# Performance work log

Hardware: AMD Instinct MI355X
Metric: run time of the kernel (lower is better)

Reference implementation:

```python
import math
import jax, jax.numpy as jnp
import numpy as np

B, H, W, C = 4, 64, 64, 96
SSM_RATIO = 2.0
D_INNER = int(SSM_RATIO * C)   # 192
D_STATE = 4
DT_RANK = math.ceil(C / 16)    # 6
K = 4                          # 4 scan directions
D_CONV = 3


def layer_norm(x, g, b, eps=1e-5):
    mu = jnp.mean(x, axis=-1, keepdims=True)
    var = jnp.var(x, axis=-1, keepdims=True)
    return (x - mu) / jnp.sqrt(var + eps) * g + b


def cross_scan(x):
    # x: (B, D, H, W) -> (B, K=4, D, L); dirs: row-major, col-major, and their reverses
    b, d, h, w = x.shape
    s0 = x.reshape(b, d, h * w)
    s1 = jnp.transpose(x, (0, 1, 3, 2)).reshape(b, d, h * w)
    return jnp.stack([s0, s1, s0[..., ::-1], s1[..., ::-1]], axis=1)


def cross_merge(ys, h, w):
    # ys: (B, K=4, D, L) -> (B, D, L); inverse of cross_scan, summed over directions
    b, k, d, L = ys.shape
    ys = ys[:, 0:2] + ys[:, 2:4][..., ::-1]
    y0 = ys[:, 0]
    y1 = jnp.transpose(ys[:, 1].reshape(b, d, w, h), (0, 1, 3, 2)).reshape(b, d, L)
    return y0 + y1


def selective_scan(u, dt, A, Bm, Cm, D4):
    # u, dt: (B,K,D,L); A: (K,D,N); Bm, Cm: (B,K,N,L); D4: (K,D)
    u_l = jnp.moveaxis(u, -1, 0)    # (L,B,K,D)
    dt_l = jnp.moveaxis(dt, -1, 0)
    B_l = jnp.moveaxis(Bm, -1, 0)   # (L,B,K,N)
    C_l = jnp.moveaxis(Cm, -1, 0)

    def step(h, inp):
        u_t, dt_t, B_t, C_t = inp
        dA = jnp.exp(dt_t[..., None] * A)                              # (B,K,D,N)
        h = h * dA + dt_t[..., None] * B_t[:, :, None, :] * u_t[..., None]
        y = jnp.sum(h * C_t[:, :, None, :], axis=-1)                   # (B,K,D)
        return h, y

    h0 = jnp.zeros(u.shape[:3] + (A.shape[-1],), u.dtype)
    _, ys = jax.lax.scan(step, h0, (u_l, dt_l, B_l, C_l))
    return jnp.moveaxis(ys, 0, -1) + D4[None, :, :, None] * u


def _block(x_rgb, x_e, in_proj_x_w, in_proj_e_w, conv_x_w, conv_x_b, conv_e_w, conv_e_b,
           x_proj_weight, dt_projs_weight, dt_projs_bias, A_logs, Ds,
           ln_r_g, ln_r_b, ln_e_g, ln_e_b, out_proj_x_w, out_proj_e_w):
    b, h, w, c = x_rgb.shape
    Din, N, R = D_INNER, D_STATE, DT_RANK

    xr = jnp.einsum('bhwc,dc->bhwd', x_rgb, in_proj_x_w)
    xe = jnp.einsum('bhwc,dc->bhwd', x_e, in_proj_e_w)
    xr = jnp.transpose(xr, (0, 3, 1, 2))  # (B,Din,H,W)
    xe = jnp.transpose(xe, (0, 3, 1, 2))

    def dwconv(x, wt, bias):
        y = jax.lax.conv_general_dilated(x, wt, (1, 1), 'SAME', feature_group_count=Din)
        return jax.nn.silu(y + bias[None, :, None, None])

    xr = dwconv(xr, conv_x_w, conv_x_b)
    xe = dwconv(xe, conv_e_w, conv_e_b)

    xs_r = cross_scan(xr)  # (B,K,Din,L)
    xs_e = cross_scan(xe)

    def proj(xs):
        dbl = jnp.einsum('bkdl,kcd->bkcl', xs, x_proj_weight)
        dtl, Bm, Cm = dbl[:, :, :R], dbl[:, :, R:R + N], dbl[:, :, R + N:]
        dtl = jnp.einsum('bkrl,kdr->bkdl', dtl, dt_projs_weight)
        dtl = jax.nn.softplus(dtl + dt_projs_bias[None, :, :, None])
        return dtl, Bm, Cm

    dt_r, B_r, C_r = proj(xs_r)
    dt_e, B_e, C_e = proj(xs_e)

    A = -jnp.exp(A_logs).reshape(K, Din, N)
    D4 = Ds.reshape(K, Din)

    # cross fusion: each modality's scan reads out through the OTHER modality's C
    y_r = selective_scan(xs_r, dt_r, A, B_r, C_e, D4)
    y_e = selective_scan(xs_e, dt_e, A, B_e, C_r, D4)

    y_r = cross_merge(y_r, h, w)  # (B,Din,L)
    y_e = cross_merge(y_e, h, w)

    y_r = layer_norm(jnp.transpose(y_r, (0, 2, 1)), ln_r_g, ln_r_b).reshape(b, h, w, Din)
    y_e = layer_norm(jnp.transpose(y_e, (0, 2, 1)), ln_e_g, ln_e_b).reshape(b, h, w, Din)

    out_r = jnp.einsum('bhwd,cd->bhwc', y_r, out_proj_x_w)
    out_e = jnp.einsum('bhwd,cd->bhwc', y_e, out_proj_e_w)

    # residual add of the wrapping block (drop_path=0, mlp_ratio=0)
    return x_rgb + out_r, x_e + out_e


def setup_inputs():
    key = jax.random.key(0)
    ks = jax.random.split(key, 16)
    N, R, Din = D_STATE, DT_RANK, D_INNER

    def rn(k, shape, s=0.02):
        return (jax.random.normal(k, shape) * s).astype(jnp.float32)

    # dt bias: inverse-softplus of dt ~ U[1e-3, 0.1]  (mamba-style init)
    dt = jnp.exp(jax.random.uniform(ks[10], (K, Din)) * (np.log(0.1) - np.log(1e-3)) + np.log(1e-3))
    dt_bias = dt + jnp.log(-jnp.expm1(-dt))

    return {
        'x_rgb': jax.random.normal(ks[0], (B, H, W, C), jnp.float32),
        'x_e': jax.random.normal(ks[1], (B, H, W, C), jnp.float32),
        'in_proj_x_w': rn(ks[2], (Din, C)),
        'in_proj_e_w': rn(ks[3], (Din, C)),
        'conv_x_w': rn(ks[4], (Din, 1, D_CONV, D_CONV), 0.1),
        'conv_x_b': jnp.zeros((Din,), jnp.float32),
        'conv_e_w': rn(ks[5], (Din, 1, D_CONV, D_CONV), 0.1),
        'conv_e_b': jnp.zeros((Din,), jnp.float32),
        'x_proj_weight': rn(ks[6], (K, R + 2 * N, Din)),
        'dt_projs_weight': rn(ks[7], (K, Din, R), R ** -0.5),
        'dt_projs_bias': dt_bias.astype(jnp.float32),
        'A_logs': jnp.log(jnp.tile(jnp.arange(1, N + 1, dtype=jnp.float32), (K * Din, 1))),
        'Ds': jnp.ones((K * Din,), jnp.float32),
        'ln_r_g': jnp.ones((Din,), jnp.float32),
        'ln_r_b': jnp.zeros((Din,), jnp.float32),
        'ln_e_g': jnp.ones((Din,), jnp.float32),
        'ln_e_b': jnp.zeros((Din,), jnp.float32),
        'out_proj_x_w': rn(ks[8], (C, Din)),
        'out_proj_e_w': rn(ks[9], (C, Din)),
    }


def reference(x_rgb, x_e, in_proj_x_w, in_proj_e_w, conv_x_w, conv_x_b, conv_e_w, conv_e_b,
              x_proj_weight, dt_projs_weight, dt_projs_bias, A_logs, Ds,
              ln_r_g, ln_r_b, ln_e_g, ln_e_b, out_proj_x_w, out_proj_e_w):
    return _block(x_rgb, x_e, in_proj_x_w, in_proj_e_w, conv_x_w, conv_x_b, conv_e_w, conv_e_b,
                  x_proj_weight, dt_projs_weight, dt_projs_bias, A_logs, Ds,
                  ln_r_g, ln_r_b, ln_e_g, ln_e_b, out_proj_x_w, out_proj_e_w)
```

## Files before the change

### kernel.cpp

```cpp
#include <hip/hip_runtime.h>

#define BB 4
#define HH 64
#define WW 64
#define CC 96
#define DIN 192
#define NS 4
#define RR 6
#define KK 4
#define LL 4096
#define NPOS (BB*LL)
#define NPD ((size_t)NPOS*DIN)
#define NDBC ((size_t)BB*KK*LL*14)
#define NCHUNK 128
#define CLEN 32
#define NCHAIN 32
#define PB 8

__device__ __forceinline__ int map_pos(int k, int l){
  switch(k){
    case 0: return l;
    case 1: { int wi=l>>6, hi=l&63; return hi*WW+wi; }
    case 2: return LL-1-l;
    default:{ int lr=LL-1-l; int wi=lr>>6, hi=lr&63; return hi*WW+wi; }
  }
}
__device__ __forceinline__ int pos_stride(int k){
  return (k==0) ? 1 : (k==1) ? WW : (k==2) ? -1 : -WW;
}

__global__ __launch_bounds__(DIN) void inproj_kernel(
    const float* __restrict__ x_rgb, const float* __restrict__ x_e,
    const float* __restrict__ w_r,   const float* __restrict__ w_e,
    float* __restrict__ xproj_r,    float* __restrict__ xproj_e){
  int blk = blockIdx.x;
  int m = blk / (NPOS/PB); int g = blk % (NPOS/PB);
  size_t rem0 = (size_t)g * PB;
  const float* x = m ? x_e : x_rgb;
  const float* w = m ? w_e : w_r;
  float* o = m ? xproj_e : xproj_r;
  __shared__ float xs[PB][CC];
  __shared__ float wt[DIN][17];
  int t = threadIdx.x;
  for(int idx=t; idx<PB*CC; idx+=DIN) xs[idx/CC][idx%CC] = x[rem0*CC + idx];
  float acc[PB];
  #pragma unroll
  for(int p=0;p<PB;p++) acc[p]=0.f;
  for(int c0=0; c0<CC; c0+=16){
    __syncthreads();
    for(int idx=t; idx<DIN*16; idx+=DIN){
      int dd = idx>>4, cc = idx&15;
      wt[dd][cc] = w[(size_t)dd*CC + c0 + cc];
    }
    __syncthreads();
    #pragma unroll
    for(int cc=0; cc<16; cc++){
      float wv = wt[t][cc];
      #pragma unroll
      for(int p=0;p<PB;p++) acc[p] += xs[p][c0+cc]*wv;
    }
  }
  #pragma unroll
  for(int p=0;p<PB;p++) o[(rem0+p)*DIN + t] = acc[p];
}

__global__ __launch_bounds__(DIN) void conv_kernel(
    const float* __restrict__ xproj_r, const float* __restrict__ xproj_e,
    const float* __restrict__ cw_r, const float* __restrict__ cb_r,
    const float* __restrict__ cw_e, const float* __restrict__ cb_e,
    float* __restrict__ xconv_r, float* __restrict__ xconv_e){
  int blk = blockIdx.x;
  int m = blk / NPOS; int rem = blk % NPOS;
  int b = rem / LL, p = rem % LL;
  int y = p >> 6, x = p & 63;
  const float* in = (m ? xproj_e : xproj_r) + (size_t)b*LL*DIN;
  const float* cw = m ? cw_e : cw_r;
  const float* cb = m ? cb_e : cb_r;
  float* out = m ? xconv_e : xconv_r;
  int d = threadIdx.x;
  float acc = cb[d];
  #pragma unroll
  for(int dy=-1;dy<=1;dy++){
    int yy = y+dy; if(yy<0 || yy>=HH) continue;
    #pragma unroll
    for(int dx=-1;dx<=1;dx++){
      int xx = x+dx; if(xx<0 || xx>=WW) continue;
      acc += in[(size_t)(yy*WW+xx)*DIN + d] * cw[d*9 + (dy+1)*3 + (dx+1)];
    }
  }
  float s = acc / (1.f + __expf(-acc));
  out[(size_t)(b*LL+p)*DIN + d] = s;
}

#define TPOS 32
__global__ __launch_bounds__(256) void projbc_kernel(
    const float* __restrict__ xconv_r, const float* __restrict__ xconv_e,
    const float* __restrict__ xpw,
    float* __restrict__ dtBC_r, float* __restrict__ dtBC_e){
  int blk = blockIdx.x;
  int m = blk / (BB*LL/TPOS); int rem = blk % (BB*LL/TPOS);
  int b = rem / (LL/TPOS); int p0 = (rem % (LL/TPOS)) * TPOS;
  const float* xc = (m ? xconv_e : xconv_r) + ((size_t)b*LL + p0)*DIN;
  float* o = (m ? dtBC_e : dtBC_r) + (size_t)b*KK*LL*14;

  __shared__ float xs[TPOS*97];
  __shared__ float wsd[56*97];

  int t = threadIdx.x;
  int g = t >> 5;
  int pl = t & 31;

  float acc[7];
  #pragma unroll
  for(int j=0;j<7;j++) acc[j]=0.f;

  for(int dt0=0; dt0<DIN; dt0+=96){
    __syncthreads();
    for(int idx=t; idx<TPOS*96; idx+=256){
      int r = idx/96, ccol = idx%96;
      xs[r*97+ccol] = xc[(size_t)r*DIN + dt0 + ccol];
    }
    for(int idx=t; idx<56*96; idx+=256){
      int r = idx/96, ccol = idx%96;
      wsd[r*97+ccol] = xpw[(size_t)r*DIN + dt0 + ccol];
    }
    __syncthreads();
    const float* xrow = &xs[pl*97];
    #pragma unroll 4
    for(int d=0; d<96; d++){
      float xv = xrow[d];
      #pragma unroll
      for(int j=0;j<7;j++) acc[j] += wsd[(g*7+j)*97 + d]*xv;
    }
  }

  int p = p0 + pl;
  int ptr_ = (p&63)*64 + (p>>6);
  #pragma unroll
  for(int j=0;j<7;j++){
    int cbar = g*7+j;
    int k = cbar/14, c = cbar%14;
    int l = (k==0) ? p : (k==1) ? ptr_ : (k==2) ? (LL-1-p) : (LL-1-ptr_);
    o[((size_t)k*LL + l)*14 + c] = acc[j];
  }
}

__global__ __launch_bounds__(DIN) void scan_p1_kernel(
    const float* __restrict__ xconv_r, const float* __restrict__ xconv_e,
    const float* __restrict__ dtBC_r, const float* __restrict__ dtBC_e,
    const float* __restrict__ dtw, const float* __restrict__ dtb,
    const float* __restrict__ A_logs,
    float* __restrict__ trans_S, float* __restrict__ sumdt){
  int ch = blockIdx.x / NCHUNK;
  int cidx = blockIdx.x % NCHUNK;
  int m = ch >> 4, b = (ch>>2)&3, k = ch&3;
  int d = threadIdx.x;
  int l0 = cidx*CLEN;

  float4 al = *(const float4*)&A_logs[(size_t)(k*DIN+d)*NS];
  float A0=-__expf(al.x), A1=-__expf(al.y), A2=-__expf(al.z), A3=-__expf(al.w);
  float Wd[RR];
  #pragma unroll
  for(int r=0;r<RR;r++) Wd[r] = dtw[((size_t)k*DIN + d)*RR + r];
  float bias = dtb[k*DIN+d];

  const float* xc    = (m ? xconv_e : xconv_r) + (size_t)b*LL*DIN;
  const float* dbc_m = (m ? dtBC_e : dtBC_r) + ((size_t)b*KK + k)*LL*14;

  __shared__ float4 db4[CLEN][4];
  __shared__ float u_s[CLEN*DIN];
  float* dbf = (float*)db4;

  for(int idx=d; idx<CLEN*14; idx+=DIN){
    int i = idx/14, j = idx%14;
    int slot = (j<6) ? (8+j) : (j-6);
    dbf[i*16+slot] = dbc_m[(size_t)l0*14 + idx];
  }
  int stride = pos_stride(k);
  int pos0 = map_pos(k, l0);
  #pragma unroll 8
  for(int i=0;i<CLEN;i++)
    u_s[i*DIN+d] = xc[(size_t)(pos0+i*stride)*DIN + d];
  __syncthreads();

  float h0=0.f,h1=0.f,h2=0.f,h3=0.f,sd=0.f;
  #pragma unroll 4
  for(int i=0;i<CLEN;i++){
    float4 Bv  = db4[i][0];
    float4 d03 = db4[i][2];
    float4 d45 = db4[i][3];
    float dtr = fmaf(d03.x,Wd[0], fmaf(d03.y,Wd[1], fmaf(d03.z,Wd[2],
                fmaf(d03.w,Wd[3], fmaf(d45.x,Wd[4], fmaf(d45.y,Wd[5], bias))))));
    float dt = fmaxf(dtr,0.f) + __logf(1.f + __expf(-fabsf(dtr)));
    sd += dt;
    float u = u_s[i*DIN + d];
    float dtu = dt*u;
    h0 = fmaf(h0, __expf(dt*A0), dtu*Bv.x);
    h1 = fmaf(h1, __expf(dt*A1), dtu*Bv.y);
    h2 = fmaf(h2, __expf(dt*A2), dtu*Bv.z);
    h3 = fmaf(h3, __expf(dt*A3), dtu*Bv.w);
  }
  size_t base = ((size_t)(ch*NCHUNK + cidx)*NS)*DIN + d;
  trans_S[base          ] = h0;
  trans_S[base +   DIN  ] = h1;
  trans_S[base + 2*DIN  ] = h2;
  trans_S[base + 3*DIN  ] = h3;
  sumdt[(size_t)(ch*NCHUNK + cidx)*DIN + d] = sd;
}

__global__ __launch_bounds__(DIN) void scan_p2_kernel(
    const float* __restrict__ trans_S, const float* __restrict__ sumdt,
    const float* __restrict__ A_logs, float* __restrict__ hin){
  int ch = blockIdx.x; int k = ch & 3; int d = threadIdx.x;
  float4 al = *(const float4*)&A_logs[(size_t)(k*DIN+d)*NS];
  float A[NS] = {-__expf(al.x), -__expf(al.y), -__expf(al.z), -__expf(al.w)};
  float h[NS] = {0.f,0.f,0.f,0.f};
  for(int c0=0;c0<NCHUNK;c0+=4){
    float S[4][NS], sdv[4];
    #pragma unroll
    for(int cc=0;cc<4;cc++){
      size_t base = ((size_t)(ch*NCHUNK + c0+cc)*NS)*DIN + d;
      #pragma unroll
      for(int n=0;n<NS;n++) S[cc][n] = trans_S[base + (size_t)n*DIN];
      sdv[cc] = sumdt[(size_t)(ch*NCHUNK + c0+cc)*DIN + d];
    }
    #pragma unroll
    for(int cc=0;cc<4;cc++){
      size_t base = ((size_t)(ch*NCHUNK + c0+cc)*NS)*DIN + d;
      #pragma unroll
      for(int n=0;n<NS;n++) hin[base + (size_t)n*DIN] = h[n];
      #pragma unroll
      for(int n=0;n<NS;n++) h[n] = fmaf(h[n], __expf(A[n]*sdv[cc]), S[cc][n]);
    }
  }
}

__global__ __launch_bounds__(DIN) void scan_p3_kernel(
    const float* __restrict__ xconv_r, const float* __restrict__ xconv_e,
    const float* __restrict__ dtBC_r, const float* __restrict__ dtBC_e,
    const float* __restrict__ dtw, const float* __restrict__ dtb,
    const float* __restrict__ A_logs, const float* __restrict__ Ds,
    const float* __restrict__ hin,
    float* __restrict__ ym_a_r, float* __restrict__ ym_a_e,
    float* __restrict__ ym_b_r, float* __restrict__ ym_b_e){
  int blk = blockIdx.x;
  int cidx = blk % NCHUNK;
  int rem  = blk / NCHUNK;
  int pg = rem & 1; rem >>= 1;
  int b  = rem & 3; int m = rem >> 2;
  int kA = pg, kB = pg + 2;
  int cidx2 = NCHUNK-1-cidx;
  int l0A = cidx*CLEN, l0B = cidx2*CLEN;

  int d = threadIdx.x;
  int st = pos_stride(kA);
  int pos0 = map_pos(kA, l0A);

  const float* xc = (m ? xconv_e : xconv_r) + (size_t)b*LL*DIN;
  const float* dbc_own = (m ? dtBC_e : dtBC_r) + (size_t)b*KK*LL*14;
  const float* dbc_oth = (m ? dtBC_r : dtBC_e) + (size_t)b*KK*LL*14;
  float* ym = (pg==0) ? (m ? ym_a_e : ym_a_r) : (m ? ym_b_e : ym_b_r);
  ym += (size_t)b*LL*DIN;

  __shared__ float4 db4A[CLEN][4];
  __shared__ float4 db4B[CLEN][4];
  __shared__ float u_s[CLEN*DIN];
  float* dbfA = (float*)db4A;
  float* dbfB = (float*)db4B;

  for(int idx=d; idx<CLEN*14; idx+=DIN){
    int i = idx/14, j = idx%14;
    int slot = (j<6) ? (8+j) : (j-6);
    dbfA[i*16+slot] = dbc_own[((size_t)kA*LL + l0A)*14 + idx];
    dbfB[i*16+slot] = dbc_own[((size_t)kB*LL + l0B)*14 + idx];
  }
  for(int idx=d; idx<CLEN*NS; idx+=DIN){
    int i = idx>>2, j = idx&3;
    dbfA[i*16 + 4 + j] = dbc_oth[((size_t)kA*LL + l0A + i)*14 + 10 + j];
    dbfB[i*16 + 4 + j] = dbc_oth[((size_t)kB*LL + l0B + i)*14 + 10 + j];
  }
  #pragma unroll 8
  for(int i=0;i<CLEN;i++)
    u_s[i*DIN+d] = xc[(size_t)(pos0+i*st)*DIN + d];
  __syncthreads();

  {
    int k = kA;
    float4 al = *(const float4*)&A_logs[(size_t)(k*DIN+d)*NS];
    float A0=-__expf(al.x), A1=-__expf(al.y), A2=-__expf(al.z), A3=-__expf(al.w);
    float Wd[RR];
    #pragma unroll
    for(int r=0;r<RR;r++) Wd[r] = dtw[((size_t)k*DIN + d)*RR + r];
    float bias = dtb[k*DIN+d];
    float Dv = Ds[k*DIN+d];
    int chA = (m*4+b)*4 + kA;
    size_t hbase = ((size_t)(chA*NCHUNK + cidx)*NS)*DIN + d;
    float h0=hin[hbase], h1=hin[hbase+DIN], h2=hin[hbase+2*DIN], h3=hin[hbase+3*DIN];
    #pragma unroll 4
    for(int i=0;i<CLEN;i++){
      float4 Bv  = db4A[i][0];
      float4 Cv  = db4A[i][1];
      float4 d03 = db4A[i][2];
      float4 d45 = db4A[i][3];
      float dtr = fmaf(d03.x,Wd[0], fmaf(d03.y,Wd[1], fmaf(d03.z,Wd[2],
                  fmaf(d03.w,Wd[3], fmaf(d45.x,Wd[4], fmaf(d45.y,Wd[5], bias))))));
      float dt = fmaxf(dtr,0.f) + __logf(1.f + __expf(-fabsf(dtr)));
      float u = u_s[i*DIN + d];
      float dtu = dt*u;
      h0 = fmaf(h0, __expf(dt*A0), dtu*Bv.x);
      h1 = fmaf(h1, __expf(dt*A1), dtu*Bv.y);
      h2 = fmaf(h2, __expf(dt*A2), dtu*Bv.z);
      h3 = fmaf(h3, __expf(dt*A3), dtu*Bv.w);
      float y = fmaf(h0,Cv.x, fmaf(h1,Cv.y, fmaf(h2,Cv.z, fmaf(h3,Cv.w, Dv*u))));
      ym[(size_t)(pos0+i*st)*DIN + d] = y;
    }
  }
  {
    int k = kB;
    float4 al = *(const float4*)&A_logs[(size_t)(k*DIN+d)*NS];
    float A0=-__expf(al.x), A1=-__expf(al.y), A2=-__expf(al.z), A3=-__expf(al.w);
    float Wd[RR];
    #pragma unroll
    for(int r=0;r<RR;r++) Wd[r] = dtw[((size_t)k*DIN + d)*RR + r];
    float bias = dtb[k*DIN+d];
    float Dv = Ds[k*DIN+d];
    int chB = (m*4+b)*4 + kB;
    size_t hbase = ((size_t)(chB*NCHUNK + cidx2)*NS)*DIN + d;
    float h0=hin[hbase], h1=hin[hbase+DIN], h2=hin[hbase+2*DIN], h3=hin[hbase+3*DIN];
    #pragma unroll 4
    for(int j=0;j<CLEN;j++){
      int pi = CLEN-1-j;
      float4 Bv  = db4B[j][0];
      float4 Cv  = db4B[j][1];
      float4 d03 = db4B[j][2];
      float4 d45 = db4B[j][3];
      float dtr = fmaf(d03.x,Wd[0], fmaf(d03.y,Wd[1], fmaf(d03.z,Wd[2],
                  fmaf(d03.w,Wd[3], fmaf(d45.x,Wd[4], fmaf(d45.y,Wd[5], bias))))));
      float dt = fmaxf(dtr,0.f) + __logf(1.f + __expf(-fabsf(dtr)));
      float u = u_s[pi*DIN + d];
      float dtu = dt*u;
      h0 = fmaf(h0, __expf(dt*A0), dtu*Bv.x);
      h1 = fmaf(h1, __expf(dt*A1), dtu*Bv.y);
      h2 = fmaf(h2, __expf(dt*A2), dtu*Bv.z);
      h3 = fmaf(h3, __expf(dt*A3), dtu*Bv.w);
      float y = fmaf(h0,Cv.x, fmaf(h1,Cv.y, fmaf(h2,Cv.z, fmaf(h3,Cv.w, Dv*u))));
      size_t a = (size_t)(pos0+pi*st)*DIN + d;
      ym[a] += y;
    }
  }
}

__global__ __launch_bounds__(DIN) void ln_out_kernel(
    const float* __restrict__ ym_a_r, const float* __restrict__ ym_a_e,
    const float* __restrict__ ym_b_r, const float* __restrict__ ym_b_e,
    const float* __restrict__ ln_rg, const float* __restrict__ ln_rb,
    const float* __restrict__ ln_eg, const float* __restrict__ ln_eb,
    const float* __restrict__ opw_r, const float* __restrict__ opw_e,
    const float* __restrict__ x_rgb, const float* __restrict__ x_e,
    float* __restrict__ out){
  int blk = blockIdx.x;
  int m = blk / (NPOS/PB); int g = blk % (NPOS/PB);
  size_t rem0 = (size_t)g * PB;
  const float* yma = (m ? ym_a_e : ym_a_r) + rem0*DIN;
  const float* ymb = (m ? ym_b_e : ym_b_r) + rem0*DIN;
  int t = threadIdx.x;
  int wid = t>>6;

  float v[PB];
  #pragma unroll
  for(int p=0;p<PB;p++) v[p] = yma[(size_t)p*DIN + t] + ymb[(size_t)p*DIN + t];

  __shared__ float red_s[PB][3], red_q[PB][3];
  #pragma unroll
  for(int p=0;p<PB;p++){
    float s = v[p], q = v[p]*v[p];
    #pragma unroll
    for(int off=32; off>0; off>>=1){ s += __shfl_down(s,off); q += __shfl_down(q,off); }
    if((t&63)==0){ red_s[p][wid]=s; red_q[p][wid]=q; }
  }
  __syncthreads();

  const float* gg = m ? ln_eg : ln_rg;
  const float* be = m ? ln_eb : ln_rb;
  __shared__ float yn_s[PB][DIN];
  float gv = gg[t], bv = be[t];
  #pragma unroll
  for(int p=0;p<PB;p++){
    float S = red_s[p][0]+red_s[p][1]+red_s[p][2];
    float Q = red_q[p][0]+red_q[p][1]+red_q[p][2];
    float mu  = S*(1.f/DIN);
    float var = Q*(1.f/DIN) - mu*mu;
    float inv = rsqrtf(var + 1e-5f);
    yn_s[p][t] = (v[p]-mu)*inv*gv + bv;
  }

  int c = t % CC;
  int pbase = t / CC;
  const float* w = (m ? opw_e : opw_r);
  __shared__ float wt[CC][17];
  float acc[4] = {0.f,0.f,0.f,0.f};
  for(int d0=0; d0<DIN; d0+=16){
    __syncthreads();
    for(int idx=t; idx<CC*16; idx+=DIN){
      int r = idx>>4, cc2 = idx&15;
      wt[r][cc2] = w[(size_t)r*DIN + d0 + cc2];
    }
    __syncthreads();
    #pragma unroll
    for(int cc2=0; cc2<16; cc2++){
      float wv = wt[c][cc2];
      int dd = d0 + cc2;
      #pragma unroll
      for(int pp=0;pp<4;pp++) acc[pp] += yn_s[pbase + 2*pp][dd]*wv;
    }
  }
  const float* xin = m ? x_e : x_rgb;
  #pragma unroll
  for(int pp=0;pp<4;pp++){
    size_t rem = rem0 + pbase + 2*pp;
    size_t oi = (size_t)m*NPOS*CC + rem*CC + c;
    out[oi] = acc[pp] + xin[rem*CC + c];
  }
}

extern "C" void kernel_launch(void* const* d_in, const int* in_sizes, int n_in,
                              void* d_out, int out_size, void* d_ws, size_t ws_size,
                              hipStream_t stream){
  const float* x_rgb = (const float*)d_in[0];
  const float* x_e   = (const float*)d_in[1];
  const float* ipw_r = (const float*)d_in[2];
  const float* ipw_e = (const float*)d_in[3];
  const float* cw_r  = (const float*)d_in[4];
  const float* cb_r  = (const float*)d_in[5];
  const float* cw_e  = (const float*)d_in[6];
  const float* cb_e  = (const float*)d_in[7];
  const float* xpw   = (const float*)d_in[8];
  const float* dtw   = (const float*)d_in[9];
  const float* dtb   = (const float*)d_in[10];
  const float* Alog  = (const float*)d_in[11];
  const float* Ds_   = (const float*)d_in[12];
  const float* ln_rg = (const float*)d_in[13];
  const float* ln_rb = (const float*)d_in[14];
  const float* ln_eg = (const float*)d_in[15];
  const float* ln_eb = (const float*)d_in[16];
  const float* opw_r = (const float*)d_in[17];
  const float* opw_e = (const float*)d_in[18];
  float* out = (float*)d_out;

  float* ws = (float*)d_ws;
  float* xproj_r = ws;
  float* xproj_e = ws + NPD;
  float* xconv_r = ws + 2*NPD;
  float* xconv_e = ws + 3*NPD;
  float* dtBC_r  = ws + 4*NPD;
  float* dtBC_e  = ws + 4*NPD + NDBC;
  float* trans_S = ws + 4*NPD + 2*NDBC;
  float* sumdt   = trans_S + (size_t)NCHAIN*NCHUNK*NS*DIN;
  float* hin     = sumdt   + (size_t)NCHAIN*NCHUNK*DIN;
  float* ym_b_r  = hin     + (size_t)NCHAIN*NCHUNK*NS*DIN;
  float* ym_b_e  = ym_b_r + NPD;
  float* ym_a_r = xproj_r;
  float* ym_a_e = xproj_e;

  inproj_kernel<<<2*NPOS/PB, DIN, 0, stream>>>(x_rgb, x_e, ipw_r, ipw_e, xproj_r, xproj_e);
  conv_kernel<<<2*NPOS, DIN, 0, stream>>>(xproj_r, xproj_e, cw_r, cb_r, cw_e, cb_e, xconv_r, xconv_e);
  projbc_kernel<<<2*BB*(LL/TPOS), 256, 0, stream>>>(xconv_r, xconv_e, xpw, dtBC_r, dtBC_e);
  scan_p1_kernel<<<NCHAIN*NCHUNK, DIN, 0, stream>>>(xconv_r, xconv_e, dtBC_r, dtBC_e,
                                                    dtw, dtb, Alog, trans_S, sumdt);
  scan_p2_kernel<<<NCHAIN, DIN, 0, stream>>>(trans_S, sumdt, Alog, hin);
  scan_p3_kernel<<<2*BB*2*NCHUNK, DIN, 0, stream>>>(xconv_r, xconv_e, dtBC_r, dtBC_e,
                                                    dtw, dtb, Alog, Ds_, hin,
                                                    ym_a_r, ym_a_e, ym_b_r, ym_b_e);
  ln_out_kernel<<<2*NPOS/PB, DIN, 0, stream>>>(ym_a_r, ym_a_e, ym_b_r, ym_b_e,
                                               ln_rg, ln_rb, ln_eg, ln_eb,
                                               opw_r, opw_e, x_rgb, x_e, out);
}
```

Measured before the change: 411.4 us.

## Restructure LN+out-proj kernel to 16 positions per block with vectorized loads

The final layernorm plus output-projection kernel now handles 16 positions per 256-thread block instead of 8 per 192-thread block. Sixteen threads cooperate on each position's layernorm using float4 loads and xor shuffles. Normalized values are stored transposed in shared memory so each thread accumulates 8 positions per output channel from float4 reads. This halves how often the weight tile is reloaded per position and cuts reduction overhead, but a quarter of the threads sit idle during the matmul phase.

```diff
diff --git a/kernel.cpp b/kernel.cpp
--- a/kernel.cpp
+++ b/kernel.cpp
@@ -16,6 +16,7 @@
 #define CLEN 32
 #define NCHAIN 32
 #define PB 8
+#define TP 16
 
 __device__ __forceinline__ int map_pos(int k, int l){
   switch(k){
@@ -350,7 +351,7 @@
   }
 }
 
-__global__ __launch_bounds__(DIN) void ln_out_kernel(
+__global__ __launch_bounds__(256) void ln_out_kernel(
     const float* __restrict__ ym_a_r, const float* __restrict__ ym_a_e,
     const float* __restrict__ ym_b_r, const float* __restrict__ ym_b_e,
     const float* __restrict__ ln_rg, const float* __restrict__ ln_rb,
@@ -359,67 +360,89 @@
     const float* __restrict__ x_rgb, const float* __restrict__ x_e,
     float* __restrict__ out){
   int blk = blockIdx.x;
-  int m = blk / (NPOS/PB); int g = blk % (NPOS/PB);
-  size_t rem0 = (size_t)g * PB;
-  const float* yma = (m ? ym_a_e : ym_a_r) + rem0*DIN;
-  const float* ymb = (m ? ym_b_e : ym_b_r) + rem0*DIN;
+  int m = blk / (NPOS/TP); int g = blk % (NPOS/TP);
+  size_t rem0 = (size_t)g * TP;
   int t = threadIdx.x;
-  int wid = t>>6;
-
-  float v[PB];
-  #pragma unroll
-  for(int p=0;p<PB;p++) v[p] = yma[(size_t)p*DIN + t] + ymb[(size_t)p*DIN + t];
-
-  __shared__ float red_s[PB][3], red_q[PB][3];
-  #pragma unroll
-  for(int p=0;p<PB;p++){
-    float s = v[p], q = v[p]*v[p];
-    #pragma unroll
-    for(int off=32; off>0; off>>=1){ s += __shfl_down(s,off); q += __shfl_down(q,off); }
-    if((t&63)==0){ red_s[p][wid]=s; red_q[p][wid]=q; }
-  }
-  __syncthreads();
-
-  const float* gg = m ? ln_eg : ln_rg;
-  const float* be = m ? ln_eb : ln_rb;
-  __shared__ float yn_s[PB][DIN];
-  float gv = gg[t], bv = be[t];
-  #pragma unroll
-  for(int p=0;p<PB;p++){
-    float S = red_s[p][0]+red_s[p][1]+red_s[p][2];
-    float Q = red_q[p][0]+red_q[p][1]+red_q[p][2];
-    float mu  = S*(1.f/DIN);
-    float var = Q*(1.f/DIN) - mu*mu;
+
+  __shared__ float yn_t[DIN][20];
+  __shared__ float wt[CC][20];
+
+  {
+    int tp = t >> 4, j = t & 15;
+    const float* yma = (m ? ym_a_e : ym_a_r) + (rem0+tp)*DIN;
+    const float* ymb = (m ? ym_b_e : ym_b_r) + (rem0+tp)*DIN;
+    float4 v4[3]; float s=0.f, q=0.f;
+    #pragma unroll
+    for(int e=0;e<3;e++){
+      float4 a4 = *(const float4*)&yma[j*12 + e*4];
+      float4 b4 = *(const float4*)&ymb[j*12 + e*4];
+      v4[e] = make_float4(a4.x+b4.x, a4.y+b4.y, a4.z+b4.z, a4.w+b4.w);
+      s += v4[e].x+v4[e].y+v4[e].z+v4[e].w;
+      q += v4[e].x*v4[e].x + v4[e].y*v4[e].y + v4[e].z*v4[e].z + v4[e].w*v4[e].w;
+    }
+    #pragma unroll
+    for(int off=8; off>0; off>>=1){ s += __shfl_xor(s,off); q += __shfl_xor(q,off); }
+    float mu  = s*(1.f/DIN);
+    float var = q*(1.f/DIN) - mu*mu;
     float inv = rsqrtf(var + 1e-5f);
-    yn_s[p][t] = (v[p]-mu)*inv*gv + bv;
+    const float* gg = m ? ln_eg : ln_rg;
+    const float* be = m ? ln_eb : ln_rb;
+    #pragma unroll
+    for(int e=0;e<3;e++){
+      int dd = j*12 + e*4;
+      float4 g4 = *(const float4*)&gg[dd];
+      float4 b4 = *(const float4*)&be[dd];
+      yn_t[dd+0][tp] = (v4[e].x-mu)*inv*g4.x + b4.x;
+      yn_t[dd+1][tp] = (v4[e].y-mu)*inv*g4.y + b4.y;
+      yn_t[dd+2][tp] = (v4[e].z-mu)*inv*g4.z + b4.z;
+      yn_t[dd+3][tp] = (v4[e].w-mu)*inv*g4.w + b4.w;
+    }
   }
 
   int c = t % CC;
   int pbase = t / CC;
   const float* w = (m ? opw_e : opw_r);
-  __shared__ float wt[CC][17];
-  float acc[4] = {0.f,0.f,0.f,0.f};
+  float acc[8];
+  #pragma unroll
+  for(int pp=0;pp<8;pp++) acc[pp]=0.f;
+
   for(int d0=0; d0<DIN; d0+=16){
     __syncthreads();
-    for(int idx=t; idx<CC*16; idx+=DIN){
+    for(int idx=t; idx<CC*16; idx+=256){
       int r = idx>>4, cc2 = idx&15;
       wt[r][cc2] = w[(size_t)r*DIN + d0 + cc2];
     }
     __syncthreads();
-    #pragma unroll
-    for(int cc2=0; cc2<16; cc2++){
-      float wv = wt[c][cc2];
-      int dd = d0 + cc2;
+    if(t < 192){
       #pragma unroll
-      for(int pp=0;pp<4;pp++) acc[pp] += yn_s[pbase + 2*pp][dd]*wv;
-    }
-  }
-  const float* xin = m ? x_e : x_rgb;
-  #pragma unroll
-  for(int pp=0;pp<4;pp++){
-    size_t rem = rem0 + pbase + 2*pp;
-    size_t oi = (size_t)m*NPOS*CC + rem*CC + c;
-    out[oi] = acc[pp] + xin[rem*CC + c];
+      for(int q4=0; q4<4; q4++){
+        float4 w4 = *(const float4*)&wt[c][q4*4];
+        #pragma unroll
+        for(int e=0;e<4;e++){
+          int dd = d0 + q4*4 + e;
+          float wv = (e==0)?w4.x:(e==1)?w4.y:(e==2)?w4.z:w4.w;
+          float4 ylo = *(const float4*)&yn_t[dd][pbase*8];
+          float4 yhi = *(const float4*)&yn_t[dd][pbase*8+4];
+          acc[0] = fmaf(ylo.x, wv, acc[0]);
+          acc[1] = fmaf(ylo.y, wv, acc[1]);
+          acc[2] = fmaf(ylo.z, wv, acc[2]);
+          acc[3] = fmaf(ylo.w, wv, acc[3]);
+          acc[4] = fmaf(yhi.x, wv, acc[4]);
+          acc[5] = fmaf(yhi.y, wv, acc[5]);
+          acc[6] = fmaf(yhi.z, wv, acc[6]);
+          acc[7] = fmaf(yhi.w, wv, acc[7]);
+        }
+      }
+    }
+  }
+  if(t < 192){
+    const float* xin = m ? x_e : x_rgb;
+    #pragma unroll
+    for(int pp=0;pp<8;pp++){
+      size_t rem = rem0 + pbase*8 + pp;
+      size_t oi = (size_t)m*NPOS*CC + rem*CC + c;
+      out[oi] = acc[pp] + xin[rem*CC + c];
+    }
   }
 }
 
@@ -471,7 +494,7 @@
   scan_p3_kernel<<<2*BB*2*NCHUNK, DIN, 0, stream>>>(xconv_r, xconv_e, dtBC_r, dtBC_e,
                                                     dtw, dtb, Alog, Ds_, hin,
                                                     ym_a_r, ym_a_e, ym_b_r, ym_b_e);
-  ln_out_kernel<<<2*NPOS/PB, DIN, 0, stream>>>(ym_a_r, ym_a_e, ym_b_r, ym_b_e,
+  ln_out_kernel<<<2*NPOS/TP, 256, 0, stream>>>(ym_a_r, ym_a_e, ym_b_r, ym_b_e,
                                                ln_rg, ln_rb, ln_eg, ln_eb,
                                                opw_r, opw_e, x_rgb, x_e, out);
 }
```

After: 384.6 us. 1.07x faster.
